# Performance work log

Measured on AMD Instinct MI355X. Metric: run time of the kernel, lower is better.

Reference implementation:

```python
import jax, jax.numpy as jnp
import numpy as np

B, T, D_IN, D_H, D_OUT = 32, 2048, 1024, 1024, 1024

def setup_inputs() -> dict:
    key = jax.random.key(0)
    k1, k2, k3, k4, k5 = jax.random.split(key, 5)
    s = jax.random.normal(k1, (B, D_IN), dtype=jnp.float32)
    h = jax.random.normal(k2, (B, T, D_H), dtype=jnp.float32)
    # params (original uses np.random.random, i.e. uniform [0,1); scale kept modest)
    W_a = jax.random.uniform(k3, (D_IN, D_OUT), dtype=jnp.float32)
    U_a = jax.random.uniform(k4, (D_H, D_OUT), dtype=jnp.float32)
    v_a = jax.random.uniform(k5, (D_OUT,), dtype=jnp.float32)
    return {"s": s, "h": h, "W_a": W_a, "U_a": U_a, "v_a": v_a}

def reference(s, h, W_a, U_a, v_a):
    # Bahdanau additive attention:
    # e_bt = v_a . tanh(s W_a + h_t U_a);  a = softmax_t(e);  c_b = sum_t a_bt h_bt
    u_a_h = jnp.einsum('bth,ho->bto', h, U_a)            # [B,T,O]
    w_a_s = jnp.einsum('bi,io->bo', s, W_a)[:, None, :]  # [B,1,O]
    e = jnp.einsum('bto,o->bt', jnp.tanh(w_a_s + u_a_h), v_a)  # [B,T]
    a = jax.nn.softmax(e, axis=-1)                       # [B,T]
    c = jnp.einsum('bt,bth->bh', a, h)                   # [B,H]
    return c
```

## Files before the change

kernel.cpp:

```cpp
#include <hip/hip_runtime.h>
#include <hip/hip_bf16.h>
#include <stdint.h>

#define Bb 32
#define Tt 2048
#define Dd 1024

typedef float    f32x4 __attribute__((ext_vector_type(4)));
typedef _Float16 f16x8 __attribute__((ext_vector_type(8)));
typedef uint32_t u32;

#define WS_A     131072
#define WS_EP    393216
#define WS_UT    4587520

__device__ __forceinline__ void gll16(const void* g, const void* lds) {
  __builtin_amdgcn_global_load_lds(
      (const __attribute__((address_space(1))) u32*)(uintptr_t)g,
      (__attribute__((address_space(3))) u32*)(uint32_t)(uintptr_t)lds,
      16, 0, 0);
}

__global__ __launch_bounds__(256) void k_ws(const float* __restrict__ s,
                                            const float* __restrict__ W,
                                            float* __restrict__ w2_ws) {
  const int b = blockIdx.x >> 2;
  const int o = (blockIdx.x & 3) * 256 + threadIdx.x;
  __shared__ float s_sh[Dd];
#pragma unroll
  for (int j = 0; j < 4; ++j)
    s_sh[threadIdx.x + 256 * j] = s[b * Dd + threadIdx.x + 256 * j];
  __syncthreads();
  float acc = 0.f;
#pragma unroll 8
  for (int i = 0; i < Dd; ++i) acc += s_sh[i] * W[(size_t)i * Dd + o];
  w2_ws[b * Dd + o] = 2.f * acc;
}

__global__ __launch_bounds__(256) void k_ut(const float* __restrict__ U,
                                            uint8_t* __restrict__ U_ts) {
  const int i0 = (blockIdx.x >> 4) * 64;
  const int o0 = (blockIdx.x & 15) * 64;
  __shared__ float tile[64][65];
  const int tx = threadIdx.x & 63;
  const int ty = threadIdx.x >> 6;
#pragma unroll
  for (int jj = 0; jj < 16; ++jj)
    tile[tx][ty + 4 * jj] = U[(size_t)(i0 + ty + 4 * jj) * Dd + o0 + tx];
  __syncthreads();
#pragma unroll
  for (int it = 0; it < 2; ++it) {
    const int g  = it * 256 + threadIdx.x;
    const int ol = g & 63;
    const int kg = g >> 6;
    const int o  = o0 + ol;
    const int k  = i0 + kg * 8;
    f16x8 r;
#pragma unroll
    for (int m = 0; m < 8; ++m) r[m] = (_Float16)tile[ol][kg * 8 + m];
    const int ob  = o >> 7, ks = k >> 6;
    const int o_l = o & 127, k_l = k & 63;
    const size_t byte = ((size_t)(ob * 16 + ks) << 14)
                      + (size_t)((k_l >> 5) * 8192 + (o_l >> 6) * 4096
                      + ((o_l >> 4) & 3) * 1024
                      + (((k_l >> 3) & 3) * 16 + (o_l & 15)) * 16);
    *(f16x8*)(U_ts + byte) = r;
  }
}

__global__ __launch_bounds__(512, 2) void k_e(const float* __restrict__ h,
                                              const uint8_t* __restrict__ U_ts,
                                              const float* __restrict__ w2_ws,
                                              const float* __restrict__ v_a,
                                              float* __restrict__ e_part) {
  const int blk = blockIdx.x;
  const int b   = blk >> 6;
  const int obb = (blk >> 4) & 3;
  const int tb  = blk & 15;
  const int tid  = threadIdx.x;
  const int lane = tid & 63;
  const int w    = tid >> 6;
  const int tw   = w >> 2;
  const int ow   = w & 3;

  __shared__ __align__(16) uint8_t Al[2][32768];
  __shared__ __align__(16) uint8_t Bl[2][16384];
  __shared__ float exch[512];

  const uint8_t* Asrc[4];
#pragma unroll
  for (int q = 0; q < 4; ++q)
    Asrc[q] = U_ts + ((size_t)((obb * 2 + (q >> 1)) * 16) << 14)
            + (size_t)(((q & 1) * 512 + w * 64 + lane) * 16);

  const float* hb[2];
  int baddr[2];
#pragma unroll
  for (int j = 0; j < 2; ++j) {
    const int u   = j * 512 + tid;
    const int t_l = u >> 3;
    const int kg  = u & 7;
    hb[j] = h + ((size_t)(b * Tt + tb * 128 + t_l)) * Dd + kg * 8;
    const int kk  = kg >> 2;
    const int klo = kg & 3;
    baddr[j] = kk * 8192 + (t_l >> 6) * 4096 + ((t_l >> 4) & 3) * 1024
             + (klo * 16 + ((t_l & 15) ^ kg)) * 16;
  }

  const int aoff = (ow >> 1) * 16384 + (ow & 1) * 4096 + lane * 16;
  const int klo_r = lane >> 4;
  const int rs0 = (klo_r * 16 + ((lane & 15) ^ klo_r)) * 16;
  const int rs1 = (klo_r * 16 + ((lane & 15) ^ klo_r ^ 4)) * 16;
  const int boff = tw * 4096;

  f32x4 acc[4][4] = {};
  f32x4 br[4];
  f16x8 pk[2];

#pragma unroll
  for (int j = 0; j < 2; ++j) {
    br[2 * j]     = *(const f32x4*)(hb[j]);
    br[2 * j + 1] = *(const f32x4*)(hb[j] + 4);
  }
#pragma unroll
  for (int q = 0; q < 4; ++q)
    gll16(Asrc[q], &Al[0][0] + q * 8192 + w * 1024);
#pragma unroll
  for (int j = 0; j < 2; ++j) {
    f16x8 t;
#pragma unroll
    for (int m2 = 0; m2 < 4; ++m2) {
      t[m2]     = (_Float16)br[2 * j][m2];
      t[4 + m2] = (_Float16)br[2 * j + 1][m2];
    }
    pk[j] = t;
    *(f16x8*)(&Bl[0][0] + baddr[j]) = t;
  }
#pragma unroll
  for (int j = 0; j < 2; ++j) {
    br[2 * j]     = *(const f32x4*)(hb[j] + 64);
    br[2 * j + 1] = *(const f32x4*)(hb[j] + 64 + 4);
  }
  asm volatile("s_waitcnt lgkmcnt(0)" ::: "memory");
  __builtin_amdgcn_sched_barrier(0);

#pragma unroll 1
  for (int ks = 0; ks < 16; ++ks) {
    const int cur = ks & 1;
    const int nxt = cur ^ 1;
    asm volatile("s_waitcnt vmcnt(4)" ::: "memory");
    __builtin_amdgcn_sched_barrier(0);
    __builtin_amdgcn_s_barrier();
    __builtin_amdgcn_sched_barrier(0);
    {
      const size_t ko = (size_t)((ks + 1) & 15) << 14;
#pragma unroll
      for (int q = 0; q < 4; ++q)
        gll16(Asrc[q] + ko, &Al[nxt][0] + q * 8192 + w * 1024);
    }
#pragma unroll
    for (int j = 0; j < 2; ++j) {
      f16x8 t;
#pragma unroll
      for (int m2 = 0; m2 < 4; ++m2) {
        t[m2]     = (_Float16)br[2 * j][m2];
        t[4 + m2] = (_Float16)br[2 * j + 1][m2];
      }
      pk[j] = t;
      *(f16x8*)(&Bl[nxt][0] + baddr[j]) = t;
    }
    {
      const int kso = ((ks + 2) & 15) * 64;
#pragma unroll
      for (int j = 0; j < 2; ++j) {
        br[2 * j]     = *(const f32x4*)(hb[j] + kso);
        br[2 * j + 1] = *(const f32x4*)(hb[j] + kso + 4);
      }
    }
    __builtin_amdgcn_sched_barrier(0);
    {
      f16x8 af[4], bf[4];
#pragma unroll
      for (int n = 0; n < 4; ++n)
        af[n] = *(const f16x8*)(&Al[cur][0] + aoff + n * 1024);
#pragma unroll
      for (int m = 0; m < 4; ++m)
        bf[m] = *(const f16x8*)(&Bl[cur][0] + boff + m * 1024 + rs0);
      asm volatile("s_waitcnt lgkmcnt(0)" ::: "memory");
      __builtin_amdgcn_sched_barrier(0);
      __builtin_amdgcn_s_setprio(1);
#pragma unroll
      for (int m = 0; m < 4; ++m)
#pragma unroll
        for (int n = 0; n < 4; ++n)
          acc[m][n] = __builtin_amdgcn_mfma_f32_16x16x32_f16(af[n], bf[m],
                                                             acc[m][n], 0, 0, 0);
      __builtin_amdgcn_s_setprio(0);
    }
    {
      f16x8 af[4], bf[4];
#pragma unroll
      for (int n = 0; n < 4; ++n)
        af[n] = *(const f16x8*)(&Al[cur][0] + aoff + 8192 + n * 1024);
#pragma unroll
      for (int m = 0; m < 4; ++m)
        bf[m] = *(const f16x8*)(&Bl[cur][0] + boff + 8192 + m * 1024 + rs1);
      asm volatile("s_waitcnt lgkmcnt(0)" ::: "memory");
      __builtin_amdgcn_sched_barrier(0);
      __builtin_amdgcn_s_setprio(1);
#pragma unroll
      for (int m = 0; m < 4; ++m)
#pragma unroll
        for (int n = 0; n < 4; ++n)
          acc[m][n] = __builtin_amdgcn_mfma_f32_16x16x32_f16(af[n], bf[m],
                                                             acc[m][n], 0, 0, 0);
      __builtin_amdgcn_s_setprio(0);
    }
  }

  const float* wbase = w2_ws + b * Dd + obb * 256;
  const float* vbase = v_a + obb * 256;
  float ep[4] = {0.f, 0.f, 0.f, 0.f};
#pragma unroll
  for (int n = 0; n < 4; ++n) {
    const int og = ow * 64 + n * 16 + ((lane >> 4) << 2);
    const f32x4 w4 = *(const f32x4*)(wbase + og);
    const f32x4 v4 = *(const f32x4*)(vbase + og);
#pragma unroll
    for (int m = 0; m < 4; ++m)
#pragma unroll
      for (int r = 0; r < 4; ++r) {
        const float x = __builtin_fmaf(acc[m][n][r], 2.f, w4[r]);
        ep[m] += v4[r] * (1.f - 2.f / (__expf(x) + 1.f));
      }
  }
#pragma unroll
  for (int m = 0; m < 4; ++m) {
    ep[m] += __shfl_xor(ep[m], 16, 64);
    ep[m] += __shfl_xor(ep[m], 32, 64);
  }
  __syncthreads();
  if (lane < 16) {
#pragma unroll
    for (int m = 0; m < 4; ++m)
      exch[ow * 128 + tw * 64 + m * 16 + lane] = ep[m];
  }
  __syncthreads();
  if (tid < 128) {
    const float sv = exch[tid] + exch[128 + tid] + exch[256 + tid] + exch[384 + tid];
    e_part[((size_t)(obb * Bb + b)) * Tt + tb * 128 + tid] = sv;
  }
}

__global__ __launch_bounds__(256) void k_sm(const float* __restrict__ e_part,
                                            float* __restrict__ a_ws) {
  const int b = blockIdx.x;
  const int lane = threadIdx.x & 63;
  const int wv = threadIdx.x >> 6;
  __shared__ float red[8];
  float ev[8];
  float m = -1e30f;
#pragma unroll
  for (int j = 0; j < 8; ++j) {
    const int t = threadIdx.x + 256 * j;
    float sv = 0.f;
#pragma unroll
    for (int o = 0; o < 4; ++o) sv += e_part[((size_t)(o * Bb + b)) * Tt + t];
    ev[j] = sv;
    m = fmaxf(m, sv);
  }
#pragma unroll
  for (int sft = 1; sft < 64; sft <<= 1) m = fmaxf(m, __shfl_xor(m, sft, 64));
  if (lane == 0) red[wv] = m;
  __syncthreads();
  m = fmaxf(fmaxf(red[0], red[1]), fmaxf(red[2], red[3]));
  float sum = 0.f;
#pragma unroll
  for (int j = 0; j < 8; ++j) { ev[j] = __expf(ev[j] - m); sum += ev[j]; }
#pragma unroll
  for (int sft = 1; sft < 64; sft <<= 1) sum += __shfl_xor(sum, sft, 64);
  if (lane == 0) red[4 + wv] = sum;
  __syncthreads();
  const float inv = 1.f / (red[4] + red[5] + red[6] + red[7]);
#pragma unroll
  for (int j = 0; j < 8; ++j) a_ws[b * Tt + threadIdx.x + 256 * j] = ev[j] * inv;
}

__global__ __launch_bounds__(256) void k_c1(const float* __restrict__ h,
                                            const float* __restrict__ a_ws,
                                            float* __restrict__ cpart) {
  const int b  = blockIdx.x >> 5;
  const int tc = blockIdx.x & 31;
  const int t0 = tc << 6;
  __shared__ float a_sh[64];
  if (threadIdx.x < 64) a_sh[threadIdx.x] = a_ws[b * Tt + t0 + threadIdx.x];
  __syncthreads();
  f32x4 acc = {0.f, 0.f, 0.f, 0.f};
  const float* hb = h + ((size_t)b * Tt + t0) * Dd + threadIdx.x * 4;
#pragma unroll 4
  for (int t = 0; t < 64; ++t) {
    const f32x4 hv = *(const f32x4*)(hb + (size_t)t * Dd);
    acc += a_sh[t] * hv;
  }
  *(f32x4*)(cpart + ((size_t)(tc * 32 + b) << 10) + threadIdx.x * 4) = acc;
}

__global__ __launch_bounds__(256) void k_c2(const float* __restrict__ cpart,
                                            float* __restrict__ out) {
  const int gid = blockIdx.x * 256 + threadIdx.x;
  const int b = gid >> 10;
  const int d = gid & 1023;
  float sv = 0.f;
#pragma unroll
  for (int tc = 0; tc < 32; ++tc) sv += cpart[((size_t)(tc * 32 + b) << 10) + d];
  out[gid] = sv;
}

extern "C" void kernel_launch(void* const* d_in, const int* in_sizes, int n_in,
                              void* d_out, int out_size, void* d_ws, size_t ws_size,
                              hipStream_t stream) {
  (void)in_sizes; (void)n_in; (void)out_size; (void)ws_size;
  const float* s  = (const float*)d_in[0];
  const float* h  = (const float*)d_in[1];
  const float* W  = (const float*)d_in[2];
  const float* U  = (const float*)d_in[3];
  const float* v  = (const float*)d_in[4];
  uint8_t* ws = (uint8_t*)d_ws;
  float*   w2_ws  = (float*)ws;
  float*   a_ws   = (float*)(ws + WS_A);
  float*   e_part = (float*)(ws + WS_EP);
  float*   cpart  = (float*)(ws + WS_EP);
  uint8_t* U_ts   = ws + WS_UT;

  k_ws<<<128, 256, 0, stream>>>(s, W, w2_ws);
  k_ut<<<256, 256, 0, stream>>>(U, U_ts);
  k_e <<<2048, 512, 0, stream>>>(h, U_ts, w2_ws, v, e_part);
  k_sm<<<Bb, 256, 0, stream>>>(e_part, a_ws);
  k_c1<<<1024, 256, 0, stream>>>(h, a_ws, cpart);
  k_c2<<<128, 256, 0, stream>>>(cpart, (float*)d_out);
}
```

Baseline: 316.4 us.

## Single-buffer LDS in attention-score GEMM to fit three blocks per CU

Replaces the double-buffered A/B LDS tiles with single buffers, roughly halving shared memory per block, and raises launch bounds from 2 to 3 blocks per CU. The pipeline is restructured so each k-step issues the A async loads and B stores, then waits in stages (vmcnt 6, then 4) so the first half of the MFMAs can start before the second half of A has landed. The intent is to trade intra-block prefetch overlap for more resident waves hiding latency, at the cost of an extra barrier per iteration and tighter register limits that could cause spills.

```diff
diff --git a/kernel.cpp b/kernel.cpp
--- a/kernel.cpp
+++ b/kernel.cpp
@@ -68,7 +68,7 @@
   }
 }
 
-__global__ __launch_bounds__(512, 2) void k_e(const float* __restrict__ h,
+__global__ __launch_bounds__(512, 3) void k_e(const float* __restrict__ h,
                                               const uint8_t* __restrict__ U_ts,
                                               const float* __restrict__ w2_ws,
                                               const float* __restrict__ v_a,
@@ -83,8 +83,8 @@
   const int tw   = w >> 2;
   const int ow   = w & 3;
 
-  __shared__ __align__(16) uint8_t Al[2][32768];
-  __shared__ __align__(16) uint8_t Bl[2][16384];
+  __shared__ __align__(16) uint8_t Al[32768];
+  __shared__ __align__(16) uint8_t Bl[16384];
   __shared__ float exch[512];
 
   const uint8_t* Asrc[4];
@@ -123,9 +123,6 @@
     br[2 * j + 1] = *(const f32x4*)(hb[j] + 4);
   }
 #pragma unroll
-  for (int q = 0; q < 4; ++q)
-    gll16(Asrc[q], &Al[0][0] + q * 8192 + w * 1024);
-#pragma unroll
   for (int j = 0; j < 2; ++j) {
     f16x8 t;
 #pragma unroll
@@ -134,29 +131,78 @@
       t[4 + m2] = (_Float16)br[2 * j + 1][m2];
     }
     pk[j] = t;
-    *(f16x8*)(&Bl[0][0] + baddr[j]) = t;
-  }
-#pragma unroll
-  for (int j = 0; j < 2; ++j) {
-    br[2 * j]     = *(const f32x4*)(hb[j] + 64);
-    br[2 * j + 1] = *(const f32x4*)(hb[j] + 64 + 4);
-  }
-  asm volatile("s_waitcnt lgkmcnt(0)" ::: "memory");
-  __builtin_amdgcn_sched_barrier(0);
+  }
 
 #pragma unroll 1
   for (int ks = 0; ks < 16; ++ks) {
-    const int cur = ks & 1;
-    const int nxt = cur ^ 1;
+    __builtin_amdgcn_sched_barrier(0);
+    __builtin_amdgcn_s_barrier();
+    __builtin_amdgcn_sched_barrier(0);
+    {
+      const size_t ko = (size_t)ks << 14;
+      gll16(Asrc[0] + ko, Al + 0 * 8192 + w * 1024);
+      gll16(Asrc[2] + ko, Al + 2 * 8192 + w * 1024);
+      __builtin_amdgcn_sched_barrier(0);
+      gll16(Asrc[1] + ko, Al + 1 * 8192 + w * 1024);
+      gll16(Asrc[3] + ko, Al + 3 * 8192 + w * 1024);
+      __builtin_amdgcn_sched_barrier(0);
+#pragma unroll
+      for (int j = 0; j < 2; ++j) *(f16x8*)(Bl + baddr[j]) = pk[j];
+      __builtin_amdgcn_sched_barrier(0);
+      const int kso = ((ks + 1) & 15) * 64;
+#pragma unroll
+      for (int j = 0; j < 2; ++j) {
+        br[2 * j]     = *(const f32x4*)(hb[j] + kso);
+        br[2 * j + 1] = *(const f32x4*)(hb[j] + kso + 4);
+      }
+      __builtin_amdgcn_sched_barrier(0);
+    }
+    asm volatile("s_waitcnt lgkmcnt(0)" ::: "memory");
+    asm volatile("s_waitcnt vmcnt(6)" ::: "memory");
+    __builtin_amdgcn_sched_barrier(0);
+    __builtin_amdgcn_s_barrier();
+    __builtin_amdgcn_sched_barrier(0);
+    {
+      f16x8 af[4], bf[4];
+#pragma unroll
+      for (int n = 0; n < 4; ++n)
+        af[n] = *(const f16x8*)(Al + aoff + n * 1024);
+#pragma unroll
+      for (int m = 0; m < 4; ++m)
+        bf[m] = *(const f16x8*)(Bl + boff + m * 1024 + rs0);
+      asm volatile("s_waitcnt lgkmcnt(0)" ::: "memory");
+      __builtin_amdgcn_sched_barrier(0);
+      __builtin_amdgcn_s_setprio(1);
+#pragma unroll
+      for (int m = 0; m < 4; ++m)
+#pragma unroll
+        for (int n = 0; n < 4; ++n)
+          acc[m][n] = __builtin_amdgcn_mfma_f32_16x16x32_f16(af[n], bf[m],
+                                                             acc[m][n], 0, 0, 0);
+      __builtin_amdgcn_s_setprio(0);
+    }
     asm volatile("s_waitcnt vmcnt(4)" ::: "memory");
     __builtin_amdgcn_sched_barrier(0);
     __builtin_amdgcn_s_barrier();
     __builtin_amdgcn_sched_barrier(0);
     {
-      const size_t ko = (size_t)((ks + 1) & 15) << 14;
-#pragma unroll
-      for (int q = 0; q < 4; ++q)
-        gll16(Asrc[q] + ko, &Al[nxt][0] + q * 8192 + w * 1024);
+      f16x8 af[4], bf[4];
+#pragma unroll
+      for (int n = 0; n < 4; ++n)
+        af[n] = *(const f16x8*)(Al + aoff + 8192 + n * 1024);
+#pragma unroll
+      for (int m = 0; m < 4; ++m)
+        bf[m] = *(const f16x8*)(Bl + boff + 8192 + m * 1024 + rs1);
+      asm volatile("s_waitcnt lgkmcnt(0)" ::: "memory");
+      __builtin_amdgcn_sched_barrier(0);
+      __builtin_amdgcn_s_setprio(1);
+#pragma unroll
+      for (int m = 0; m < 4; ++m)
+#pragma unroll
+        for (int n = 0; n < 4; ++n)
+          acc[m][n] = __builtin_amdgcn_mfma_f32_16x16x32_f16(af[n], bf[m],
+                                                             acc[m][n], 0, 0, 0);
+      __builtin_amdgcn_s_setprio(0);
     }
 #pragma unroll
     for (int j = 0; j < 2; ++j) {
@@ -167,54 +213,6 @@
         t[4 + m2] = (_Float16)br[2 * j + 1][m2];
       }
       pk[j] = t;
-      *(f16x8*)(&Bl[nxt][0] + baddr[j]) = t;
-    }
-    {
-      const int kso = ((ks + 2) & 15) * 64;
-#pragma unroll
-      for (int j = 0; j < 2; ++j) {
-        br[2 * j]     = *(const f32x4*)(hb[j] + kso);
-        br[2 * j + 1] = *(const f32x4*)(hb[j] + kso + 4);
-      }
-    }
-    __builtin_amdgcn_sched_barrier(0);
-    {
-      f16x8 af[4], bf[4];
-#pragma unroll
-      for (int n = 0; n < 4; ++n)
-        af[n] = *(const f16x8*)(&Al[cur][0] + aoff + n * 1024);
-#pragma unroll
-      for (int m = 0; m < 4; ++m)
-        bf[m] = *(const f16x8*)(&Bl[cur][0] + boff + m * 1024 + rs0);
-      asm volatile("s_waitcnt lgkmcnt(0)" ::: "memory");
-      __builtin_amdgcn_sched_barrier(0);
-      __builtin_amdgcn_s_setprio(1);
-#pragma unroll
-      for (int m = 0; m < 4; ++m)
-#pragma unroll
-        for (int n = 0; n < 4; ++n)
-          acc[m][n] = __builtin_amdgcn_mfma_f32_16x16x32_f16(af[n], bf[m],
-                                                             acc[m][n], 0, 0, 0);
-      __builtin_amdgcn_s_setprio(0);
-    }
-    {
-      f16x8 af[4], bf[4];
-#pragma unroll
-      for (int n = 0; n < 4; ++n)
-        af[n] = *(const f16x8*)(&Al[cur][0] + aoff + 8192 + n * 1024);
-#pragma unroll
-      for (int m = 0; m < 4; ++m)
-        bf[m] = *(const f16x8*)(&Bl[cur][0] + boff + 8192 + m * 1024 + rs1);
-      asm volatile("s_waitcnt lgkmcnt(0)" ::: "memory");
-      __builtin_amdgcn_sched_barrier(0);
-      __builtin_amdgcn_s_setprio(1);
-#pragma unroll
-      for (int m = 0; m < 4; ++m)
-#pragma unroll
-        for (int n = 0; n < 4; ++n)
-          acc[m][n] = __builtin_amdgcn_mfma_f32_16x16x32_f16(af[n], bf[m],
-                                                             acc[m][n], 0, 0, 0);
-      __builtin_amdgcn_s_setprio(0);
     }
   }
 
```

Measured after the change: 312.5 us. About the same (-1.2%).
